# Optimization experiments

Measured on AMD Instinct MI355X. Metric: run time of the kernel, lower is better.

## Reference

```python
import jax, jax.numpy as jnp
import numpy as np

D = 768        # d_model
NH = 12        # n_head
HD = D // NH   # head_dim = 64
T = 8          # num_frames
SCALE = 1.0
LN_EPS = 1e-5


def _layer_norm(x, g, b):
    # fp16-safe LayerNorm: compute in fp32, cast back (matches LayerNorm subclass)
    x32 = x.astype(jnp.float32)
    mu = jnp.mean(x32, axis=-1, keepdims=True)
    var = jnp.mean(jnp.square(x32 - mu), axis=-1, keepdims=True)
    y = (x32 - mu) / jnp.sqrt(var + LN_EPS) * g + b
    return y.astype(x.dtype)


def _adapter(x, w1, b1, w2, b2):
    # Adapter with skip_connect=False: fc1 -> exact GELU -> fc2
    h = jax.nn.gelu(x @ w1.T + b1, approximate=False)
    return h @ w2.T + b2


def _mha(xq, ykv, w_in, b_in, w_out, b_out, need_weights=False):
    # xq: (Tx, N, D), ykv: (Ty, N, D); manual in-proj split like the torch code
    q = xq @ w_in[:D].T + b_in[:D]
    k = ykv @ w_in[D:2 * D].T + b_in[D:2 * D]
    v = ykv @ w_in[2 * D:].T + b_in[2 * D:]
    Tx, N = q.shape[0], q.shape[1]
    Ty = k.shape[0]
    q = q.reshape(Tx, N, NH, HD).transpose(1, 2, 0, 3)  # (N, H, Tx, hd)
    k = k.reshape(Ty, N, NH, HD).transpose(1, 2, 0, 3)
    v = v.reshape(Ty, N, NH, HD).transpose(1, 2, 0, 3)
    aff = jnp.einsum('nhqd,nhkd->nhqk', q, k) / jnp.asarray(HD ** 0.5, q.dtype)
    if need_weights:
        # torch does this under no_grad: sum over heads, exp, sum over (Tx*Ty)
        w = jax.lax.stop_gradient(
            jnp.sum(jnp.exp(jnp.sum(aff, axis=1)).reshape(N, -1), axis=-1))
    p = jax.nn.softmax(aff, axis=-1)
    out = jnp.einsum('nhqk,nhkd->nhqd', p, v)
    out = out.transpose(2, 0, 1, 3).reshape(Tx, N, D)
    out = out @ w_out.T + b_out
    if need_weights:
        return out, w
    return out


def setup_inputs() -> dict:
    key = jax.random.key(0)
    ks = jax.random.split(key, 12)
    DH = D // 4  # adapter hidden = 192

    def w(k, shape):
        return jax.random.normal(k, shape, jnp.float32) * 0.02

    z = lambda *s: jnp.zeros(s, jnp.float32)
    return {
        'x': jax.random.normal(ks[0], (197, 64, D), jnp.float32),
        'in_proj_w': w(ks[1], (3 * D, D)), 'in_proj_b': z(3 * D),
        'out_proj_w': w(ks[2], (D, D)), 'out_proj_b': z(D),
        'ln1_g': jnp.ones((D,), jnp.float32), 'ln1_b': z(D),
        'ln2_g': jnp.ones((D,), jnp.float32), 'ln2_b': z(D),
        'fc_w': w(ks[3], (4 * D, D)), 'fc_b': z(4 * D),
        'proj_w': w(ks[4], (D, 4 * D)), 'proj_b': z(D),
        'sa1_w': w(ks[5], (DH, D)), 'sa1_b': z(DH),
        'sa2_w': w(ks[6], (D, DH)), 'sa2_b': z(D),
        'ta1_w': w(ks[7], (DH, D)), 'ta1_b': z(DH),
        'ta2_w': w(ks[8], (D, DH)), 'ta2_b': z(D),
        'ma1_w': w(ks[9], (DH, D)), 'ma1_b': z(DH),
        'ma2_w': w(ks[10], (D, DH)), 'ma2_b': z(D),
    }


def reference(x, in_proj_w, in_proj_b, out_proj_w, out_proj_b,
              ln1_g, ln1_b, ln2_g, ln2_b, fc_w, fc_b, proj_w, proj_b,
              sa1_w, sa1_b, sa2_w, sa2_b, ta1_w, ta1_b, ta2_w, ta2_b,
              ma1_w, ma1_b, ma2_w, ma2_b):
    n, bt, d = x.shape
    b = bt // T
    # temporal attention on the class token: 'n (b t) d -> t (b n) d'
    ct = x[0]                                   # (bt, d)
    xt = ct.reshape(b, T, d).transpose(1, 0, 2)  # (T, b, d)
    xt = _mha(_layer_norm(xt, ln1_g, ln1_b), _layer_norm(xt, ln1_g, ln1_b),
              in_proj_w, in_proj_b, out_proj_w, out_proj_b)
    xt = _adapter(xt, ta1_w, ta1_b, ta2_w, ta2_b)
    xt = xt.transpose(1, 0, 2).reshape(1, bt, d)  # 't (b n) d -> n (b t) d'

    xln = _layer_norm(x, ln1_g, ln1_b)
    ori_attn, ori_w = _mha(xln, xln, in_proj_w, in_proj_b,
                           out_proj_w, out_proj_b, need_weights=True)
    crs_attn, crs_w = _mha(xln, xt, in_proj_w, in_proj_b,
                           out_proj_w, out_proj_b, need_weights=True)
    lam = (crs_w / (crs_w + ori_w))[None, :, None]  # (1, bt, 1)
    x = x + (1.0 - lam) * ori_attn \
          + SCALE * _adapter(lam * crs_attn, sa1_w, sa1_b, sa2_w, sa2_b)

    xn = _layer_norm(x, ln2_g, ln2_b)
    h = xn @ fc_w.T + fc_b
    h = h * jax.nn.sigmoid(1.702 * h)  # QuickGELU
    mlp_out = h @ proj_w.T + proj_b
    x = x + mlp_out + SCALE * _adapter(xn, ma1_w, ma1_b, ma2_w, ma2_b)
    return x
```

## Files before the change

kernel.cpp:

```cpp
#include <hip/hip_runtime.h>
#include <hip/hip_bf16.h>
#include <math.h>


typedef __attribute__((ext_vector_type(8))) short bf16x8;
typedef __attribute__((ext_vector_type(4))) float f32x4;

__device__ __forceinline__ float bf2f(short s) {
  unsigned u = ((unsigned)(unsigned short)s) << 16;
  float f;
  __builtin_memcpy(&f, &u, 4);
  return f;
}
__device__ __forceinline__ short f2bf(float f) {
  __hip_bfloat16 h = __float2bfloat16(f);
  short s;
  __builtin_memcpy(&s, &h, 2);
  return s;
}

__device__ __forceinline__ void gld16(void* lds, const void* g) {
  __builtin_amdgcn_global_load_lds(
      (const __attribute__((address_space(1))) unsigned int*)g,
      (__attribute__((address_space(3))) unsigned int*)lds, 16, 0, 0);
}

struct WPair { const float* s; short* d; int n; };
struct WArr { WPair p[10]; };

__global__ __launch_bounds__(256)
void convert_k(WArr a) {
  WPair w = a.p[blockIdx.y];
  for (int i = blockIdx.x * 256 + threadIdx.x; i < w.n; i += gridDim.x * 256)
    w.d[i] = f2bf(w.s[i]);
}

__global__ __launch_bounds__(256)
void ln_k(const float* __restrict__ in, const float* __restrict__ g,
          const float* __restrict__ b, short* __restrict__ out) {
  const int t = blockIdx.x;
  const float* xr = in + (size_t)t * 768;
  const int tid = threadIdx.x;
  float v0 = xr[tid], v1 = xr[tid + 256], v2 = xr[tid + 512];
  float s = v0 + v1 + v2;
#pragma unroll
  for (int m = 1; m < 64; m <<= 1) s += __shfl_xor(s, m);
  __shared__ float red[4];
  if ((tid & 63) == 0) red[tid >> 6] = s;
  __syncthreads();
  float mu = (red[0] + red[1] + red[2] + red[3]) * (1.f / 768.f);
  __syncthreads();
  float d0 = v0 - mu, d1 = v1 - mu, d2 = v2 - mu;
  float q = d0 * d0 + d1 * d1 + d2 * d2;
#pragma unroll
  for (int m = 1; m < 64; m <<= 1) q += __shfl_xor(q, m);
  if ((tid & 63) == 0) red[tid >> 6] = q;
  __syncthreads();
  float rstd = rsqrtf((red[0] + red[1] + red[2] + red[3]) * (1.f / 768.f) + 1e-5f);
  size_t o = (size_t)t * 768;
  out[o + tid]       = f2bf(d0 * rstd * g[tid]       + b[tid]);
  out[o + tid + 256] = f2bf(d1 * rstd * g[tid + 256] + b[tid + 256]);
  out[o + tid + 512] = f2bf(d2 * rstd * g[tid + 512] + b[tid + 512]);
}

template <int ACT, int EPI>
__global__ __launch_bounds__(256)
void gemm_k(const short* __restrict__ A, int lda,
            const short* __restrict__ W,
            const float* __restrict__ bias,
            short* __restrict__ outb, float* __restrict__ outf,
            const float* __restrict__ lam,
            int M, int N, int K) {
  __shared__ short As[64][40];
  __shared__ short Ws[64][40];
  const int tid = threadIdx.x;
  const int n0 = blockIdx.x * 64;
  const int m0 = blockIdx.y * 64;
  const int lane = tid & 63, w = tid >> 6;
  const int wr = w >> 1, wc = w & 1;
  const int g = lane >> 4, li = lane & 15;
  const int srow = tid >> 2, scol = (tid & 3) * 8;

  f32x4 acc[2][2];
#pragma unroll
  for (int i = 0; i < 2; i++)
#pragma unroll
    for (int j = 0; j < 2; j++) acc[i][j] = (f32x4){0.f, 0.f, 0.f, 0.f};

  const short* Aptr = A + (size_t)(m0 + srow) * lda + scol;
  const short* Wptr = W + (size_t)(n0 + srow) * K + scol;

  for (int kk = 0; kk < K; kk += 32) {
    __syncthreads();
    *(bf16x8*)&As[srow][scol] = *(const bf16x8*)(Aptr + kk);
    *(bf16x8*)&Ws[srow][scol] = *(const bf16x8*)(Wptr + kk);
    __syncthreads();
    bf16x8 a[2], b[2];
#pragma unroll
    for (int mi = 0; mi < 2; ++mi)
      a[mi] = *(const bf16x8*)&As[wr * 32 + mi * 16 + li][g * 8];
#pragma unroll
    for (int ni = 0; ni < 2; ++ni)
      b[ni] = *(const bf16x8*)&Ws[wc * 32 + ni * 16 + li][g * 8];
#pragma unroll
    for (int mi = 0; mi < 2; ++mi)
#pragma unroll
      for (int ni = 0; ni < 2; ++ni)
        acc[mi][ni] = __builtin_amdgcn_mfma_f32_16x16x32_bf16(
            a[mi], b[ni], acc[mi][ni], 0, 0, 0);
  }

#pragma unroll
  for (int mi = 0; mi < 2; ++mi)
#pragma unroll
    for (int ni = 0; ni < 2; ++ni)
#pragma unroll
      for (int r = 0; r < 4; ++r) {
        int row = m0 + wr * 32 + mi * 16 + g * 4 + r;
        int col = n0 + wc * 32 + ni * 16 + li;
        float v = acc[mi][ni][r];
        if (bias) v += bias[col];
        if (ACT == 1) v = v / (1.f + __expf(-1.702f * v));
        if (ACT == 2) v = 0.5f * v * (1.f + erff(v * 0.70710678118f));
        size_t idx = (size_t)row * N + col;
        if (EPI == 0) outb[idx] = f2bf(v);
        else if (EPI == 1) outf[idx] = v;
        else if (EPI == 5) outb[idx] = f2bf(v * lam[row]);
      }
}

template <int ACT, int EPI>
__global__ __launch_bounds__(256, 4)
void gemm128p_k(const short* __restrict__ A, int lda,
                const short* __restrict__ W,
                const float* __restrict__ bias,
                short* __restrict__ outb, float* __restrict__ outf,
                const float* __restrict__ lam,
                const float* __restrict__ addv,
                const float* __restrict__ resid,
                const short* __restrict__ A2, int lda2,
                const short* __restrict__ W2,
                const float* __restrict__ bias2, int K2,
                int M, int N, int K, int nx) {
  int nwg = gridDim.x;
  int orig = blockIdx.x;
  int q = nwg >> 3, r = nwg & 7;
  int xcd = orig & 7, cidx = orig >> 3;
  int wgid = (xcd < r ? xcd * (q + 1) : r * (q + 1) + (xcd - r) * q) + cidx;
  const int n0 = (wgid % nx) * 128;
  const int m0 = (wgid / nx) * 128;

  __shared__ short As[2][128][32];
  __shared__ short Ws[2][128][32];
  const int tid = threadIdx.x;
  const int w = tid >> 6, lane = tid & 63;
  const int g = lane >> 4, li = lane & 15;
  const int wr = w >> 1, wc = w & 1;

  const int srow = w * 16 + (lane >> 2);
  const int scol = ((lane & 3) ^ ((lane >> 3) & 3)) * 8;
  const int cxr  = (g ^ ((li >> 1) & 3)) * 8;

  f32x4 acc[4][4];
#pragma unroll
  for (int i = 0; i < 4; i++)
#pragma unroll
    for (int j = 0; j < 4; j++) acc[i][j] = (f32x4){0.f, 0.f, 0.f, 0.f};

  int ar0 = m0 + srow;       if (ar0 > M - 1) ar0 = M - 1;
  int ar1 = m0 + 64 + srow;  if (ar1 > M - 1) ar1 = M - 1;
  const short* Ap0 = A + (size_t)ar0 * lda + scol;
  const short* Ap1 = A + (size_t)ar1 * lda + scol;
  const short* Wp0 = W + (size_t)(n0 + srow) * K + scol;
  const short* Wp1 = W + (size_t)(n0 + 64 + srow) * K + scol;
  const short* A2b = A2 ? A2 : A;
  const short* W2b = W2 ? W2 : W;
  const short* Bp0 = A2b + (size_t)ar0 * lda2 + scol;
  const short* Bp1 = A2b + (size_t)ar1 * lda2 + scol;
  const short* Vp0 = W2b + (size_t)(n0 + srow) * K2 + scol;
  const short* Vp1 = W2b + (size_t)(n0 + 64 + srow) * K2 + scol;

  const int ks1 = K >> 5;
  const int ks2 = A2 ? (K2 >> 5) : 0;
  const int total = ks1 + ks2;

  auto STAGE = [&](int s, int bi) {
    if (s < ks1) {
      const int kk = s * 32;
      gld16(&As[bi][w * 16][0],      Ap0 + kk);
      gld16(&As[bi][64 + w * 16][0], Ap1 + kk);
      gld16(&Ws[bi][w * 16][0],      Wp0 + kk);
      gld16(&Ws[bi][64 + w * 16][0], Wp1 + kk);
    } else {
      const int kk = (s - ks1) * 32;
      gld16(&As[bi][w * 16][0],      Bp0 + kk);
      gld16(&As[bi][64 + w * 16][0], Bp1 + kk);
      gld16(&Ws[bi][w * 16][0],      Vp0 + kk);
      gld16(&Ws[bi][64 + w * 16][0], Vp1 + kk);
    }
  };

  STAGE(0, 0);

  for (int t = 0; t < total; ++t) {
    const int bi = t & 1;
    if (t + 1 < total) {
      STAGE(t + 1, bi ^ 1);
      asm volatile("s_waitcnt vmcnt(4)" ::: "memory");
    } else {
      asm volatile("s_waitcnt vmcnt(0)" ::: "memory");
    }
    __builtin_amdgcn_s_barrier();

    bf16x8 a[4], b[4];
#pragma unroll
    for (int mi = 0; mi < 4; ++mi)
      a[mi] = *(const bf16x8*)&As[bi][wr * 64 + mi * 16 + li][cxr];
#pragma unroll
    for (int ni = 0; ni < 4; ++ni)
      b[ni] = *(const bf16x8*)&Ws[bi][wc * 64 + ni * 16 + li][cxr];
    asm volatile("s_waitcnt lgkmcnt(0)" ::: "memory");
    __builtin_amdgcn_sched_barrier(0);
#pragma unroll
    for (int mi = 0; mi < 4; ++mi)
#pragma unroll
      for (int ni = 0; ni < 4; ++ni)
        acc[mi][ni] = __builtin_amdgcn_mfma_f32_16x16x32_bf16(
            a[mi], b[ni], acc[mi][ni], 0, 0, 0);
    __builtin_amdgcn_s_barrier();
  }

#pragma unroll
  for (int mi = 0; mi < 4; ++mi)
#pragma unroll
    for (int ni = 0; ni < 4; ++ni)
#pragma unroll
      for (int r = 0; r < 4; ++r) {
        int row = m0 + wr * 64 + mi * 16 + g * 4 + r;
        int col = n0 + wc * 64 + ni * 16 + li;
        if (row >= M) continue;
        float v = acc[mi][ni][r];
        if (bias) v += bias[col];
        if (bias2) v += bias2[col];
        if (ACT == 1) v = v / (1.f + __expf(-1.702f * v));
        if (ACT == 2) v = 0.5f * v * (1.f + erff(v * 0.70710678118f));
        size_t idx = (size_t)row * N + col;
        if (EPI == 0) outb[idx] = f2bf(v);
        else if (EPI == 2) {
          float l = lam[row & 63];
          outf[idx] = resid[idx] + (1.f - l) * v + addv[(size_t)(row & 63) * 768 + col];
        } else if (EPI == 6) outf[idx] = resid[idx] + v;
      }
}

template <int ACT, int EPI>
__global__ __launch_bounds__(256, 4)
void gemm64n_k(const short* __restrict__ A, int lda,
               const short* __restrict__ W,
               const float* __restrict__ bias,
               short* __restrict__ outb, float* __restrict__ outf,
               const float* __restrict__ lam,
               const float* __restrict__ addv,
               const float* __restrict__ resid,
               const short* __restrict__ A2, int lda2,
               const short* __restrict__ W2,
               const float* __restrict__ bias2, int K2,
               int M, int N, int K, int nx) {
  int nwg = gridDim.x;
  int orig = blockIdx.x;
  int q = nwg >> 3, r = nwg & 7;
  int xcd = orig & 7, cidx = orig >> 3;
  int wgid = (xcd < r ? xcd * (q + 1) : r * (q + 1) + (xcd - r) * q) + cidx;
  const int n0 = (wgid % nx) * 64;
  const int m0 = (wgid / nx) * 128;

  __shared__ short As[2][128][32];
  __shared__ short Ws[2][64][32];
  const int tid = threadIdx.x;
  const int w = tid >> 6, lane = tid & 63;
  const int g = lane >> 4, li = lane & 15;

  const int srow = w * 16 + (lane >> 2);
  const int scol = ((lane & 3) ^ ((lane >> 3) & 3)) * 8;
  const int cxr  = (g ^ ((li >> 1) & 3)) * 8;

  f32x4 acc[2][4];
#pragma unroll
  for (int i = 0; i < 2; i++)
#pragma unroll
    for (int j = 0; j < 4; j++) acc[i][j] = (f32x4){0.f, 0.f, 0.f, 0.f};

  int ar0 = m0 + srow;       if (ar0 > M - 1) ar0 = M - 1;
  int ar1 = m0 + 64 + srow;  if (ar1 > M - 1) ar1 = M - 1;
  const short* Ap0 = A + (size_t)ar0 * lda + scol;
  const short* Ap1 = A + (size_t)ar1 * lda + scol;
  const short* Wp0 = W + (size_t)(n0 + srow) * K + scol;
  const short* A2b = A2 ? A2 : A;
  const short* W2b = W2 ? W2 : W;
  const short* Bp0 = A2b + (size_t)ar0 * lda2 + scol;
  const short* Bp1 = A2b + (size_t)ar1 * lda2 + scol;
  const short* Vp0 = W2b + (size_t)(n0 + srow) * K2 + scol;

  const int ks1 = K >> 5;
  const int ks2 = A2 ? (K2 >> 5) : 0;
  const int total = ks1 + ks2;

  auto STAGE = [&](int s, int bi) {
    if (s < ks1) {
      const int kk = s * 32;
      gld16(&As[bi][w * 16][0],      Ap0 + kk);
      gld16(&As[bi][64 + w * 16][0], Ap1 + kk);
      gld16(&Ws[bi][w * 16][0],      Wp0 + kk);
    } else {
      const int kk = (s - ks1) * 32;
      gld16(&As[bi][w * 16][0],      Bp0 + kk);
      gld16(&As[bi][64 + w * 16][0], Bp1 + kk);
      gld16(&Ws[bi][w * 16][0],      Vp0 + kk);
    }
  };

  STAGE(0, 0);

  for (int t = 0; t < total; ++t) {
    const int bi = t & 1;
    if (t + 1 < total) {
      STAGE(t + 1, bi ^ 1);
      asm volatile("s_waitcnt vmcnt(3)" ::: "memory");
    } else {
      asm volatile("s_waitcnt vmcnt(0)" ::: "memory");
    }
    __builtin_amdgcn_s_barrier();

    bf16x8 a[2], b[4];
#pragma unroll
    for (int mi = 0; mi < 2; ++mi)
      a[mi] = *(const bf16x8*)&As[bi][w * 32 + mi * 16 + li][cxr];
#pragma unroll
    for (int ni = 0; ni < 4; ++ni)
      b[ni] = *(const bf16x8*)&Ws[bi][ni * 16 + li][cxr];
    asm volatile("s_waitcnt lgkmcnt(0)" ::: "memory");
    __builtin_amdgcn_sched_barrier(0);
#pragma unroll
    for (int mi = 0; mi < 2; ++mi)
#pragma unroll
      for (int ni = 0; ni < 4; ++ni)
        acc[mi][ni] = __builtin_amdgcn_mfma_f32_16x16x32_bf16(
            a[mi], b[ni], acc[mi][ni], 0, 0, 0);
    __builtin_amdgcn_s_barrier();
  }

#pragma unroll
  for (int mi = 0; mi < 2; ++mi)
#pragma unroll
    for (int ni = 0; ni < 4; ++ni)
#pragma unroll
      for (int r = 0; r < 4; ++r) {
        int row = m0 + w * 32 + mi * 16 + g * 4 + r;
        int col = n0 + ni * 16 + li;
        if (row >= M) continue;
        float v = acc[mi][ni][r];
        if (bias) v += bias[col];
        if (bias2) v += bias2[col];
        if (ACT == 1) v = v / (1.f + __expf(-1.702f * v));
        if (ACT == 2) v = 0.5f * v * (1.f + erff(v * 0.70710678118f));
        size_t idx = (size_t)row * N + col;
        if (EPI == 0) outb[idx] = f2bf(v);
        else if (EPI == 2) {
          float l = lam[row & 63];
          outf[idx] = resid[idx] + (1.f - l) * v + addv[(size_t)(row & 63) * 768 + col];
        } else if (EPI == 6) outf[idx] = resid[idx] + v;
      }
}

__global__ __launch_bounds__(256)
void attn_k(const short* __restrict__ qkv, short* __restrict__ attn_out) {
  const int n = blockIdx.x;
  const int h = blockIdx.y;
  const int tid = threadIdx.x;
  const int lane = tid & 63, w = tid >> 6;
  const int g = lane >> 4, li = lane & 15;

  __shared__ short Vt[64][232];
  __shared__ short Pl[4][16][232];

  {
    const int d = tid & 63;
    for (int key = tid >> 6; key < 224; key += 4) {
      short v = 0;
      if (key < 197)
        v = qkv[(size_t)(key * 64 + n) * 2304 + 1536 + h * 64 + d];
      Vt[d][key] = v;
    }
  }
  __syncthreads();

  const short* Qb = qkv + (size_t)n * 2304 + h * 64;
  const short* Kb = Qb + 768;

  for (int mt = w; mt < 13; mt += 4) {
    const int m0 = mt * 16;
    int arow = m0 + li;
    if (arow > 196) arow = 196;
    bf16x8 a0 = *(const bf16x8*)(Qb + (size_t)arow * 147456 + g * 8);
    bf16x8 a1 = *(const bf16x8*)(Qb + (size_t)arow * 147456 + 32 + g * 8);

    float s[13][4];
#pragma unroll
    for (int nt = 0; nt < 13; ++nt) {
      int kc = nt * 16 + li;
      if (kc > 196) kc = 196;
      bf16x8 b0 = *(const bf16x8*)(Kb + (size_t)kc * 147456 + g * 8);
      bf16x8 b1 = *(const bf16x8*)(Kb + (size_t)kc * 147456 + 32 + g * 8);
      f32x4 acc = (f32x4){0.f, 0.f, 0.f, 0.f};
      acc = __builtin_amdgcn_mfma_f32_16x16x32_bf16(a0, b0, acc, 0, 0, 0);
      acc = __builtin_amdgcn_mfma_f32_16x16x32_bf16(a1, b1, acc, 0, 0, 0);
#pragma unroll
      for (int r = 0; r < 4; ++r) s[nt][r] = acc[r] * 0.125f;
    }

#pragma unroll
    for (int r = 0; r < 4; ++r) {
      float mx = -1e30f;
#pragma unroll
      for (int nt = 0; nt < 13; ++nt) {
        if (nt * 16 + li >= 197) s[nt][r] = -1e30f;
        mx = fmaxf(mx, s[nt][r]);
      }
      mx = fmaxf(mx, __shfl_xor(mx, 1));
      mx = fmaxf(mx, __shfl_xor(mx, 2));
      mx = fmaxf(mx, __shfl_xor(mx, 4));
      mx = fmaxf(mx, __shfl_xor(mx, 8));
      float sum = 0.f;
#pragma unroll
      for (int nt = 0; nt < 13; ++nt) {
        float e = (s[nt][r] <= -1e29f) ? 0.f : __expf(s[nt][r] - mx);
        s[nt][r] = e;
        sum += e;
      }
      sum += __shfl_xor(sum, 1);
      sum += __shfl_xor(sum, 2);
      sum += __shfl_xor(sum, 4);
      sum += __shfl_xor(sum, 8);
      float inv = 1.f / sum;
#pragma unroll
      for (int nt = 0; nt < 13; ++nt) s[nt][r] *= inv;
    }

#pragma unroll
    for (int r = 0; r < 4; ++r) {
      int row = g * 4 + r;
#pragma unroll
      for (int nt = 0; nt < 13; ++nt)
        Pl[w][row][nt * 16 + li] = f2bf(s[nt][r]);
      Pl[w][row][208 + li] = 0;
    }
    asm volatile("s_waitcnt lgkmcnt(0)" ::: "memory");
    __builtin_amdgcn_sched_barrier(0);

    f32x4 o[4];
#pragma unroll
    for (int ni = 0; ni < 4; ++ni) o[ni] = (f32x4){0.f, 0.f, 0.f, 0.f};
#pragma unroll
    for (int kk = 0; kk < 7; ++kk) {
      bf16x8 pa = *(const bf16x8*)&Pl[w][li][kk * 32 + g * 8];
#pragma unroll
      for (int ni = 0; ni < 4; ++ni) {
        bf16x8 vb = *(const bf16x8*)&Vt[ni * 16 + li][kk * 32 + g * 8];
        o[ni] = __builtin_amdgcn_mfma_f32_16x16x32_bf16(pa, vb, o[ni], 0, 0, 0);
      }
    }
#pragma unroll
    for (int ni = 0; ni < 4; ++ni)
#pragma unroll
      for (int r = 0; r < 4; ++r) {
        int prow = m0 + g * 4 + r;
        if (prow < 197)
          attn_out[(size_t)(prow * 64 + n) * 768 + h * 64 + ni * 16 + li] =
              f2bf(o[ni][r]);
      }
  }
}

__global__ __launch_bounds__(256)
void lam_part_k(const short* __restrict__ qkv, float* __restrict__ eo_part) {
  const int n = blockIdx.x;
  const int mt = blockIdx.y;
  const int tid = threadIdx.x;
  const int lane = tid & 63, w = tid >> 6;
  const int g = lane >> 4, li = lane & 15;
  const short* Qb = qkv + (size_t)n * 2304;
  const short* Kb = Qb + 768;

  int arow = mt * 16 + li;
  if (arow > 196) arow = 196;
  const short* Ap = Qb + (size_t)arow * 147456;

  bf16x8 a[24];
#pragma unroll
  for (int s = 0; s < 24; ++s)
    a[s] = *(const bf16x8*)(Ap + s * 32 + g * 8);

  float eo = 0.f;
  for (int nt = w; nt < 13; nt += 4) {
    int kc = nt * 16 + li;
    if (kc > 196) kc = 196;
    const short* Bp = Kb + (size_t)kc * 147456;
    f32x4 acc = (f32x4){0.f, 0.f, 0.f, 0.f};
#pragma unroll
    for (int s = 0; s < 24; ++s) {
      bf16x8 b = *(const bf16x8*)(Bp + s * 32 + g * 8);
      acc = __builtin_amdgcn_mfma_f32_16x16x32_bf16(a[s], b, acc, 0, 0, 0);
    }
#pragma unroll
    for (int r = 0; r < 4; ++r) {
      int prow = mt * 16 + g * 4 + r;
      int col = nt * 16 + li;
      if (prow < 197 && col < 197) eo += __expf(acc[r] * 0.125f);
    }
  }

#pragma unroll
  for (int m = 1; m < 64; m <<= 1) eo += __shfl_xor(eo, m);
  __shared__ float red[4];
  if (lane == 0) red[w] = eo;
  __syncthreads();
  if (tid == 0)
    eo_part[n * 13 + mt] = red[0] + red[1] + red[2] + red[3];
}

__global__ __launch_bounds__(64)
void lam_fin_k(const short* __restrict__ qkv, const short* __restrict__ kvt,
               const float* __restrict__ eo_part, float* __restrict__ lam) {
  const int n = blockIdx.x;
  const int lane = threadIdx.x;
  const short* kt = kvt + (size_t)n * 1536;

  float ec = 0.f;
  for (int p = lane; p < 197; p += 64) {
    const short* qp = qkv + (size_t)n * 2304 + (size_t)p * 147456;
    float dot = 0.f;
    for (int d0 = 0; d0 < 768; d0 += 8) {
      bf16x8 qa = *(const bf16x8*)(qp + d0);
      bf16x8 ka = *(const bf16x8*)(kt + d0);
#pragma unroll
      for (int j = 0; j < 8; ++j) dot += bf2f(qa[j]) * bf2f(ka[j]);
    }
    ec += __expf(dot * 0.125f);
  }
#pragma unroll
  for (int m = 1; m < 64; m <<= 1) ec += __shfl_xor(ec, m);

  if (lane == 0) {
    float eo = 0.f;
#pragma unroll
    for (int t = 0; t < 13; ++t) eo += eo_part[n * 13 + t];
    lam[n] = ec / (ec + eo);
  }
}

__global__ __launch_bounds__(64)
void tattn_k(const short* __restrict__ qkv, short* __restrict__ attn_t) {
  const int bb = blockIdx.x, h = blockIdx.y;
  const int tid = threadIdx.x;
  __shared__ float sm[8][9];
  {
    const int tt = tid >> 3, ss = tid & 7;
    const short* q = qkv + (size_t)(bb * 8 + tt) * 2304 + h * 64;
    const short* k = qkv + (size_t)(bb * 8 + ss) * 2304 + 768 + h * 64;
    float dot = 0.f;
#pragma unroll
    for (int d = 0; d < 64; d += 8) {
      bf16x8 qa = *(const bf16x8*)(q + d);
      bf16x8 ka = *(const bf16x8*)(k + d);
#pragma unroll
      for (int j = 0; j < 8; ++j) dot += bf2f(qa[j]) * bf2f(ka[j]);
    }
    sm[tt][ss] = dot * 0.125f;
  }
  __syncthreads();
  if (tid < 8) {
    float mx = -1e30f;
#pragma unroll
    for (int s2 = 0; s2 < 8; ++s2) mx = fmaxf(mx, sm[tid][s2]);
    float sum = 0.f;
#pragma unroll
    for (int s2 = 0; s2 < 8; ++s2) {
      float e = __expf(sm[tid][s2] - mx);
      sm[tid][s2] = e;
      sum += e;
    }
    float inv = 1.f / sum;
#pragma unroll
    for (int s2 = 0; s2 < 8; ++s2) sm[tid][s2] *= inv;
  }
  __syncthreads();
  {
    const int d = tid;
    float v[8];
#pragma unroll
    for (int s2 = 0; s2 < 8; ++s2)
      v[s2] = bf2f(qkv[(size_t)(bb * 8 + s2) * 2304 + 1536 + h * 64 + d]);
#pragma unroll
    for (int tt = 0; tt < 8; ++tt) {
      float o = 0.f;
#pragma unroll
      for (int s2 = 0; s2 < 8; ++s2) o += sm[tt][s2] * v[s2];
      attn_t[(size_t)(bb * 8 + tt) * 768 + h * 64 + d] = f2bf(o);
    }
  }
}

extern "C" void kernel_launch(void* const* d_in, const int* in_sizes, int n_in,
                              void* d_out, int out_size, void* d_ws,
                              size_t ws_size, hipStream_t stream) {
  (void)in_sizes; (void)n_in; (void)out_size; (void)ws_size;

  const float* x          = (const float*)d_in[0];
  const float* in_proj_w  = (const float*)d_in[1];
  const float* in_proj_b  = (const float*)d_in[2];
  const float* out_proj_w = (const float*)d_in[3];
  const float* out_proj_b = (const float*)d_in[4];
  const float* ln1_g      = (const float*)d_in[5];
  const float* ln1_b      = (const float*)d_in[6];
  const float* ln2_g      = (const float*)d_in[7];
  const float* ln2_b      = (const float*)d_in[8];
  const float* fc_w       = (const float*)d_in[9];
  const float* fc_b       = (const float*)d_in[10];
  const float* proj_w     = (const float*)d_in[11];
  const float* proj_b     = (const float*)d_in[12];
  const float* sa1_w      = (const float*)d_in[13];
  const float* sa1_b      = (const float*)d_in[14];
  const float* sa2_w      = (const float*)d_in[15];
  const float* sa2_b      = (const float*)d_in[16];
  const float* ta1_w      = (const float*)d_in[17];
  const float* ta1_b      = (const float*)d_in[18];
  const float* ta2_w      = (const float*)d_in[19];
  const float* ta2_b      = (const float*)d_in[20];
  const float* ma1_w      = (const float*)d_in[21];
  const float* ma1_b      = (const float*)d_in[22];
  const float* ma2_w      = (const float*)d_in[23];
  const float* ma2_b      = (const float*)d_in[24];

  char* ws = (char*)d_ws;
  short* xln  = (short*)(ws + 0);
  short* qkv  = (short*)(ws + 19365888);
  short* hbuf = (short*)(ws + 0);
  short* attn = (short*)(ws + 77463552);
  short* h2   = (short*)(ws + 77463552);
  float* x1   = (float*)(ws + 96829440);
  short* xn   = (short*)(ws + 135561216);

  char* wreg = ws + 154927104;
  short* w_inproj  = (short*)(wreg + 0);
  short* w_outproj = (short*)(wreg + 3538944);
  short* w_fc      = (short*)(wreg + 4718592);
  short* w_proj    = (short*)(wreg + 9437184);
  short* w_sa1     = (short*)(wreg + 14155776);
  short* w_sa2     = (short*)(wreg + 14450688);
  short* w_ta1     = (short*)(wreg + 14745600);
  short* w_ta2     = (short*)(wreg + 15040512);
  short* w_ma1     = (short*)(wreg + 15335424);
  short* w_ma2     = (short*)(wreg + 15630336);

  char* sm = ws + 170852352;
  short* attn_t  = (short*)(sm + 0);
  short* tproj   = (short*)(sm + 98304);
  short* th      = (short*)(sm + 196608);
  short* xt_out  = (short*)(sm + 221184);
  short* kv_t    = (short*)(sm + 319488);
  short* a_in    = (short*)(sm + 516096);
  short* sa_h    = (short*)(sm + 614400);
  float* sa_out  = (float*)(sm + 638976);
  float* lam     = (float*)(sm + 835584);
  float* eo_part = (float*)(sm + 835840);

  float* out = (float*)d_out;

  WArr arr;
  arr.p[0] = {in_proj_w,  w_inproj,  2304 * 768};
  arr.p[1] = {out_proj_w, w_outproj, 768 * 768};
  arr.p[2] = {fc_w,       w_fc,      3072 * 768};
  arr.p[3] = {proj_w,     w_proj,    768 * 3072};
  arr.p[4] = {sa1_w,      w_sa1,     192 * 768};
  arr.p[5] = {sa2_w,      w_sa2,     768 * 192};
  arr.p[6] = {ta1_w,      w_ta1,     192 * 768};
  arr.p[7] = {ta2_w,      w_ta2,     768 * 192};
  arr.p[8] = {ma1_w,      w_ma1,     192 * 768};
  arr.p[9] = {ma2_w,      w_ma2,     768 * 192};
  convert_k<<<dim3(128, 10), 256, 0, stream>>>(arr);

  ln_k<<<12608, 256, 0, stream>>>(x, ln1_g, ln1_b, xln);

  gemm128p_k<0, 0><<<18 * 99, 256, 0, stream>>>(
      xln, 768, w_inproj, in_proj_b, qkv, nullptr, nullptr, nullptr, nullptr,
      nullptr, 0, nullptr, nullptr, 32, 12608, 2304, 768, 18);

  lam_part_k<<<dim3(64, 13), 256, 0, stream>>>(qkv, eo_part);

  tattn_k<<<dim3(8, 12), 64, 0, stream>>>(qkv, attn_t);

  gemm_k<0, 0><<<dim3(12, 1), 256, 0, stream>>>(
      attn_t, 768, w_outproj, out_proj_b, tproj, nullptr, nullptr, 64, 768, 768);
  gemm_k<2, 0><<<dim3(3, 1), 256, 0, stream>>>(
      tproj, 768, w_ta1, ta1_b, th, nullptr, nullptr, 64, 192, 768);
  gemm_k<0, 0><<<dim3(12, 1), 256, 0, stream>>>(
      th, 192, w_ta2, ta2_b, xt_out, nullptr, nullptr, 64, 768, 192);
  gemm_k<0, 0><<<dim3(24, 1), 256, 0, stream>>>(
      xt_out, 768, w_inproj + 768 * 768, in_proj_b + 768, kv_t, nullptr,
      nullptr, 64, 1536, 768);

  attn_k<<<dim3(64, 12), 256, 0, stream>>>(qkv, attn);

  lam_fin_k<<<64, 64, 0, stream>>>(qkv, kv_t, eo_part, lam);

  gemm_k<0, 5><<<dim3(12, 1), 256, 0, stream>>>(
      kv_t + 768, 1536, w_outproj, out_proj_b, a_in, nullptr, lam, 64, 768, 768);
  gemm_k<2, 0><<<dim3(3, 1), 256, 0, stream>>>(
      a_in, 768, w_sa1, sa1_b, sa_h, nullptr, nullptr, 64, 192, 768);
  gemm_k<0, 1><<<dim3(12, 1), 256, 0, stream>>>(
      sa_h, 192, w_sa2, sa2_b, nullptr, sa_out, nullptr, 64, 768, 192);

  gemm64n_k<0, 2><<<12 * 99, 256, 0, stream>>>(
      attn, 768, w_outproj, out_proj_b, nullptr, x1, lam, sa_out, x,
      nullptr, 0, nullptr, nullptr, 32, 12608, 768, 768, 12);

  ln_k<<<12608, 256, 0, stream>>>(x1, ln2_g, ln2_b, xn);

  gemm128p_k<1, 0><<<24 * 99, 256, 0, stream>>>(
      xn, 768, w_fc, fc_b, hbuf, nullptr, nullptr, nullptr, nullptr,
      nullptr, 0, nullptr, nullptr, 32, 12608, 3072, 768, 24);
  gemm_k<2, 0><<<dim3(3, 197), 256, 0, stream>>>(
      xn, 768, w_ma1, ma1_b, h2, nullptr, nullptr, 12608, 192, 768);

  gemm64n_k<0, 6><<<12 * 99, 256, 0, stream>>>(
      hbuf, 3072, w_proj, proj_b, nullptr, out, nullptr, nullptr, x1,
      h2, 192, w_ma2, ma2_b, 192, 12608, 768, 3072, 12);
}
```

Measured before the change: 690.9 us.

## Widen N-tile to 128 and add triple-buffered LDS pipeline in projection GEMMs

The 64-column GEMM kernel used for the out-projection and MLP down-projection becomes a 128x128 tile kernel. Each wave now computes a 64x64 subtile with 16 MFMAs per K-step, which raises operand reuse and halves the grid to 594 workgroups. The LDS double buffer is replaced by a three-stage ring that prefetches two steps ahead and drops the trailing barrier. The larger accumulators and LDS footprint may lower occupancy, and fewer workgroups means less parallelism across the 256 CUs.

```diff
diff --git a/kernel.cpp b/kernel.cpp
--- a/kernel.cpp
+++ b/kernel.cpp
@@ -255,38 +255,39 @@
 
 template <int ACT, int EPI>
 __global__ __launch_bounds__(256, 4)
-void gemm64n_k(const short* __restrict__ A, int lda,
-               const short* __restrict__ W,
-               const float* __restrict__ bias,
-               short* __restrict__ outb, float* __restrict__ outf,
-               const float* __restrict__ lam,
-               const float* __restrict__ addv,
-               const float* __restrict__ resid,
-               const short* __restrict__ A2, int lda2,
-               const short* __restrict__ W2,
-               const float* __restrict__ bias2, int K2,
-               int M, int N, int K, int nx) {
+void gemm128q_k(const short* __restrict__ A, int lda,
+                const short* __restrict__ W,
+                const float* __restrict__ bias,
+                short* __restrict__ outb, float* __restrict__ outf,
+                const float* __restrict__ lam,
+                const float* __restrict__ addv,
+                const float* __restrict__ resid,
+                const short* __restrict__ A2, int lda2,
+                const short* __restrict__ W2,
+                const float* __restrict__ bias2, int K2,
+                int M, int N, int K, int nx) {
   int nwg = gridDim.x;
   int orig = blockIdx.x;
   int q = nwg >> 3, r = nwg & 7;
   int xcd = orig & 7, cidx = orig >> 3;
   int wgid = (xcd < r ? xcd * (q + 1) : r * (q + 1) + (xcd - r) * q) + cidx;
-  const int n0 = (wgid % nx) * 64;
+  const int n0 = (wgid % nx) * 128;
   const int m0 = (wgid / nx) * 128;
 
-  __shared__ short As[2][128][32];
-  __shared__ short Ws[2][64][32];
+  __shared__ short As[3][128][32];
+  __shared__ short Ws[3][128][32];
   const int tid = threadIdx.x;
   const int w = tid >> 6, lane = tid & 63;
   const int g = lane >> 4, li = lane & 15;
+  const int wr = w >> 1, wc = w & 1;
 
   const int srow = w * 16 + (lane >> 2);
   const int scol = ((lane & 3) ^ ((lane >> 3) & 3)) * 8;
   const int cxr  = (g ^ ((li >> 1) & 3)) * 8;
 
-  f32x4 acc[2][4];
-#pragma unroll
-  for (int i = 0; i < 2; i++)
+  f32x4 acc[4][4];
+#pragma unroll
+  for (int i = 0; i < 4; i++)
 #pragma unroll
     for (int j = 0; j < 4; j++) acc[i][j] = (f32x4){0.f, 0.f, 0.f, 0.f};
 
@@ -295,11 +296,13 @@
   const short* Ap0 = A + (size_t)ar0 * lda + scol;
   const short* Ap1 = A + (size_t)ar1 * lda + scol;
   const short* Wp0 = W + (size_t)(n0 + srow) * K + scol;
+  const short* Wp1 = W + (size_t)(n0 + 64 + srow) * K + scol;
   const short* A2b = A2 ? A2 : A;
   const short* W2b = W2 ? W2 : W;
   const short* Bp0 = A2b + (size_t)ar0 * lda2 + scol;
   const short* Bp1 = A2b + (size_t)ar1 * lda2 + scol;
   const short* Vp0 = W2b + (size_t)(n0 + srow) * K2 + scol;
+  const short* Vp1 = W2b + (size_t)(n0 + 64 + srow) * K2 + scol;
 
   const int ks1 = K >> 5;
   const int ks2 = A2 ? (K2 >> 5) : 0;
@@ -311,52 +314,57 @@
       gld16(&As[bi][w * 16][0],      Ap0 + kk);
       gld16(&As[bi][64 + w * 16][0], Ap1 + kk);
       gld16(&Ws[bi][w * 16][0],      Wp0 + kk);
+      gld16(&Ws[bi][64 + w * 16][0], Wp1 + kk);
     } else {
       const int kk = (s - ks1) * 32;
       gld16(&As[bi][w * 16][0],      Bp0 + kk);
       gld16(&As[bi][64 + w * 16][0], Bp1 + kk);
       gld16(&Ws[bi][w * 16][0],      Vp0 + kk);
+      gld16(&Ws[bi][64 + w * 16][0], Vp1 + kk);
     }
   };
 
   STAGE(0, 0);
-
+  if (total > 1) STAGE(1, 1);
+
+  int bi = 0, pb = 2;
   for (int t = 0; t < total; ++t) {
-    const int bi = t & 1;
-    if (t + 1 < total) {
-      STAGE(t + 1, bi ^ 1);
-      asm volatile("s_waitcnt vmcnt(3)" ::: "memory");
-    } else {
+    if (t + 1 < total)
+      asm volatile("s_waitcnt vmcnt(4)" ::: "memory");
+    else
       asm volatile("s_waitcnt vmcnt(0)" ::: "memory");
-    }
     __builtin_amdgcn_s_barrier();
 
-    bf16x8 a[2], b[4];
-#pragma unroll
-    for (int mi = 0; mi < 2; ++mi)
-      a[mi] = *(const bf16x8*)&As[bi][w * 32 + mi * 16 + li][cxr];
+    if (t + 2 < total) STAGE(t + 2, pb);
+
+    bf16x8 a[4], b[4];
+#pragma unroll
+    for (int mi = 0; mi < 4; ++mi)
+      a[mi] = *(const bf16x8*)&As[bi][wr * 64 + mi * 16 + li][cxr];
 #pragma unroll
     for (int ni = 0; ni < 4; ++ni)
-      b[ni] = *(const bf16x8*)&Ws[bi][ni * 16 + li][cxr];
+      b[ni] = *(const bf16x8*)&Ws[bi][wc * 64 + ni * 16 + li][cxr];
     asm volatile("s_waitcnt lgkmcnt(0)" ::: "memory");
     __builtin_amdgcn_sched_barrier(0);
 #pragma unroll
-    for (int mi = 0; mi < 2; ++mi)
+    for (int mi = 0; mi < 4; ++mi)
 #pragma unroll
       for (int ni = 0; ni < 4; ++ni)
         acc[mi][ni] = __builtin_amdgcn_mfma_f32_16x16x32_bf16(
             a[mi], b[ni], acc[mi][ni], 0, 0, 0);
-    __builtin_amdgcn_s_barrier();
-  }
-
-#pragma unroll
-  for (int mi = 0; mi < 2; ++mi)
+
+    bi = bi + 1; if (bi == 3) bi = 0;
+    pb = pb + 1; if (pb == 3) pb = 0;
+  }
+
+#pragma unroll
+  for (int mi = 0; mi < 4; ++mi)
 #pragma unroll
     for (int ni = 0; ni < 4; ++ni)
 #pragma unroll
       for (int r = 0; r < 4; ++r) {
-        int row = m0 + w * 32 + mi * 16 + g * 4 + r;
-        int col = n0 + ni * 16 + li;
+        int row = m0 + wr * 64 + mi * 16 + g * 4 + r;
+        int col = n0 + wc * 64 + ni * 16 + li;
         if (row >= M) continue;
         float v = acc[mi][ni][r];
         if (bias) v += bias[col];
@@ -720,9 +728,9 @@
   gemm_k<0, 1><<<dim3(12, 1), 256, 0, stream>>>(
       sa_h, 192, w_sa2, sa2_b, nullptr, sa_out, nullptr, 64, 768, 192);
 
-  gemm64n_k<0, 2><<<12 * 99, 256, 0, stream>>>(
+  gemm128q_k<0, 2><<<6 * 99, 256, 0, stream>>>(
       attn, 768, w_outproj, out_proj_b, nullptr, x1, lam, sa_out, x,
-      nullptr, 0, nullptr, nullptr, 32, 12608, 768, 768, 12);
+      nullptr, 0, nullptr, nullptr, 32, 12608, 768, 768, 6);
 
   ln_k<<<12608, 256, 0, stream>>>(x1, ln2_g, ln2_b, xn);
 
@@ -732,7 +740,7 @@
   gemm_k<2, 0><<<dim3(3, 197), 256, 0, stream>>>(
       xn, 768, w_ma1, ma1_b, h2, nullptr, nullptr, 12608, 192, 768);
 
-  gemm64n_k<0, 6><<<12 * 99, 256, 0, stream>>>(
+  gemm128q_k<0, 6><<<6 * 99, 256, 0, stream>>>(
       hbuf, 3072, w_proj, proj_b, nullptr, out, nullptr, nullptr, x1,
-      h2, 192, w_ma2, ma2_b, 192, 12608, 768, 3072, 12);
-}
+      h2, 192, w_ma2, ma2_b, 192, 12608, 768, 3072, 6);
+}
```

New measurement: 688.7 us. About the same (-0.3%).
